# Kernel tuning notes

Measured on AMD Instinct MI355X. Metric: run time of the kernel, lower is better.

The kernel has to match this reference:

```python
import jax, jax.numpy as jnp
import numpy as np

N_AB, N_AG, F = 20000, 20000, 256
E_AB, E_AG, E_D = 320000, 320000, 640000
EPS = 1e-5


def _bn(x, gamma, beta):
    # BatchNorm1d, training-mode batch statistics (deterministic), biased variance
    mu = x.mean(0)
    var = x.var(0)
    return (x - mu) * jax.lax.rsqrt(var + EPS) * gamma + beta


def _gcn(x, ei, W, b, n):
    # PyG GCNConv: add self loops, symmetric deg^-1/2 normalization, scatter-add
    loop = jnp.arange(n, dtype=ei.dtype)
    src = jnp.concatenate([ei[0], loop])
    dst = jnp.concatenate([ei[1], loop])
    deg = jax.ops.segment_sum(jnp.ones_like(src, dtype=x.dtype), dst, num_segments=n)
    dinv = jax.lax.rsqrt(jnp.maximum(deg, 1.0))  # deg >= 1 due to self loops
    norm = dinv[src] * dinv[dst]                 # [E]
    h = x @ W                                    # [n, D]
    return jax.ops.segment_sum(h[src] * norm[:, None], dst, num_segments=n) + b


def _gat(x, ei, W, a_s, a_d, b, n, slope=0.2):
    # PyG GATConv, heads=1, add self loops; attention dropout off (eval mode)
    loop = jnp.arange(n, dtype=ei.dtype)
    src = jnp.concatenate([ei[0], loop])
    dst = jnp.concatenate([ei[1], loop])
    h = x @ W                                    # [n, D]
    e = jax.nn.leaky_relu((h @ a_s)[src] + (h @ a_d)[dst], slope)  # [E]
    # segment softmax over incoming edges of each dst node
    m = jax.ops.segment_max(e, dst, num_segments=n)
    ex = jnp.exp(e - m[dst])
    s = jax.ops.segment_sum(ex, dst, num_segments=n)
    alpha = ex / s[dst]
    return jax.ops.segment_sum(h[src] * alpha[:, None], dst, num_segments=n) + b


def setup_inputs() -> dict:
    key = jax.random.key(0)
    ks = jax.random.split(key, 20)
    sc = 1.0 / np.sqrt(F)
    sc2 = 1.0 / np.sqrt(2 * F)
    inp = {
        "x_ab": jax.random.normal(ks[0], (N_AB, F), jnp.float32),
        "x_ag": jax.random.normal(ks[1], (N_AG, F), jnp.float32),
        "W_gcn": jax.random.normal(ks[2], (F, F), jnp.float32) * sc,
        "b_gcn": jnp.zeros((F,), jnp.float32),
        "g1": jnp.ones((F,), jnp.float32),
        "be1": jnp.zeros((F,), jnp.float32),
        "W_aggcn": jax.random.normal(ks[3], (F, F), jnp.float32) * sc,
        "b_aggcn": jnp.zeros((F,), jnp.float32),
        "ag_g1": jnp.ones((F,), jnp.float32),
        "ag_be1": jnp.zeros((F,), jnp.float32),
        "W_gat": jax.random.normal(ks[4], (F, F), jnp.float32) * sc,
        "a_src": jax.random.normal(ks[5], (F,), jnp.float32) * sc,
        "a_dst": jax.random.normal(ks[6], (F,), jnp.float32) * sc,
        "b_gat": jnp.zeros((F,), jnp.float32),
        "W_gat2": jax.random.normal(ks[7], (F, F), jnp.float32) * sc,
        "a_src2": jax.random.normal(ks[8], (F,), jnp.float32) * sc,
        "a_dst2": jax.random.normal(ks[9], (F,), jnp.float32) * sc,
        "b_gat2": jnp.zeros((F,), jnp.float32),
        "ag_g2": jnp.ones((2 * F,), jnp.float32),
        "ag_be2": jnp.zeros((2 * F,), jnp.float32),
        "W_agfc": jax.random.normal(ks[10], (2 * F, 1), jnp.float32) * sc2,
        "b_agfc": jnp.zeros((1,), jnp.float32),
        "g2": jnp.ones((2 * F,), jnp.float32),
        "be2": jnp.zeros((2 * F,), jnp.float32),
        "W_fc": jax.random.normal(ks[11], (2 * F, 1), jnp.float32) * sc2,
        "b_fc": jnp.zeros((1,), jnp.float32),
        "edge_x_ab": jax.random.randint(ks[12], (2, E_AB), 0, N_AB, jnp.int32),
        "edge_x_ag": jax.random.randint(ks[13], (2, E_AG), 0, N_AG, jnp.int32),
        "edge_index_d": jax.random.randint(ks[14], (2, E_D), 0, N_AB + N_AG, jnp.int32),
    }
    return inp


def reference(x_ab, x_ag, W_gcn, b_gcn, g1, be1, W_aggcn, b_aggcn, ag_g1, ag_be1,
              W_gat, a_src, a_dst, b_gat, W_gat2, a_src2, a_dst2, b_gat2,
              ag_g2, ag_be2, W_agfc, b_agfc, g2, be2, W_fc, b_fc,
              edge_x_ab, edge_x_ag, edge_index_d):
    relu = jax.nn.relu
    h_ab = relu(_bn(_gcn(x_ab, edge_x_ab, W_gcn, b_gcn, N_AB), g1, be1))
    h_ag = relu(_bn(_gcn(x_ag, edge_x_ag, W_aggcn, b_aggcn, N_AG), ag_g1, ag_be1))
    # dropout layers are identity in eval mode
    n = N_AB + N_AG
    x = jnp.concatenate([h_ab, h_ag], axis=0)
    x = relu(_gat(x, edge_index_d, W_gat, a_src, a_dst, b_gat, n))
    x = _gat(x, edge_index_d, W_gat2, a_src2, a_dst2, b_gat2, n)
    x1, x2 = x[:N_AB], x[N_AB:]
    out_ag = relu(_bn(jnp.concatenate([x2, h_ag], axis=1), ag_g2, ag_be2)) @ W_agfc + b_agfc
    out_ab = relu(_bn(jnp.concatenate([x1, h_ab], axis=1), g2, be2)) @ W_fc + b_fc
    return out_ab, out_ag
```

## Files before the change

kernel.cpp:

```cpp
#include <hip/hip_runtime.h>
#include <hip/hip_bf16.h>
#include <stdint.h>

#define NF 256
#define EPSV 1e-5f
#define PB 160
#define MAXBUK 160

typedef unsigned short u16;
typedef unsigned int u32;
typedef short short8 __attribute__((ext_vector_type(8)));
typedef float floatx4 __attribute__((ext_vector_type(4)));

#define P_BGCN 0
#define P_G1 256
#define P_BE1 512
#define P_BAGG 768
#define P_AGG1 1024
#define P_AGBE1 1280
#define P_ASRC 1536
#define P_ADST 1792
#define P_BGAT 2048
#define P_ASRC2 2304
#define P_ADST2 2560
#define P_BGAT2 2816
#define P_G2 3072
#define P_BE2 3584
#define P_WFC 4096
#define P_AGG2 4608
#define P_AGBE2 5120
#define P_WAGFC 5632
#define P_BFC 6144
#define P_BAGFC 6145

__device__ __forceinline__ float bf2f(u16 u) {
    union { unsigned int i; float f; } v; v.i = ((unsigned int)u) << 16; return v.f;
}
__device__ __forceinline__ u16 f2bf(float f) {
    unsigned int x = __float_as_uint(f);
    unsigned int r = x + 0x7fffu + ((x >> 16) & 1u);
    return (u16)(r >> 16);
}
__device__ __forceinline__ float sane(float f) {
    return (f == f && fabsf(f) < 1e30f) ? f : 0.f;
}
__device__ __forceinline__ unsigned int zap2(unsigned int w) {
    if ((w & 0x00007F80u) == 0x00007F80u) w &= 0xFFFF0000u;
    if ((w & 0x7F800000u) == 0x7F800000u) w &= 0x0000FFFFu;
    return w;
}
__device__ __forceinline__ float lrelu(float x) { return x > 0.f ? x : 0.2f * x; }

__device__ __forceinline__ float4 ld4h(const u16* p) {
    uint2 u = *(const uint2*)p;
    float4 r;
    r.x = bf2f((u16)(u.x & 0xFFFFu)); r.y = bf2f((u16)(u.x >> 16));
    r.z = bf2f((u16)(u.y & 0xFFFFu)); r.w = bf2f((u16)(u.y >> 16));
    return r;
}
__device__ __forceinline__ void st4h(u16* p, float4 v) {
    uint2 u;
    u.x = (unsigned)f2bf(v.x) | ((unsigned)f2bf(v.y) << 16);
    u.y = (unsigned)f2bf(v.z) | ((unsigned)f2bf(v.w) << 16);
    *(uint2*)p = u;
}

__device__ __forceinline__ void fma8(const uint4 u, float a, float* acc) {
    acc[0] = fmaf(__uint_as_float(u.x << 16), a, acc[0]);
    acc[1] = fmaf(__uint_as_float(u.x & 0xFFFF0000u), a, acc[1]);
    acc[2] = fmaf(__uint_as_float(u.y << 16), a, acc[2]);
    acc[3] = fmaf(__uint_as_float(u.y & 0xFFFF0000u), a, acc[3]);
    acc[4] = fmaf(__uint_as_float(u.z << 16), a, acc[4]);
    acc[5] = fmaf(__uint_as_float(u.z & 0xFFFF0000u), a, acc[5]);
    acc[6] = fmaf(__uint_as_float(u.w << 16), a, acc[6]);
    acc[7] = fmaf(__uint_as_float(u.w & 0xFFFF0000u), a, acc[7]);
}
__device__ __forceinline__ void st8h(u16* p, const float* v) {
    uint4 u;
    u.x = (u32)f2bf(v[0]) | ((u32)f2bf(v[1]) << 16);
    u.y = (u32)f2bf(v[2]) | ((u32)f2bf(v[3]) << 16);
    u.z = (u32)f2bf(v[4]) | ((u32)f2bf(v[5]) << 16);
    u.w = (u32)f2bf(v[6]) | ((u32)f2bf(v[7]) << 16);
    *(uint4*)p = u;
}

__device__ __forceinline__ float wredsum(float v) {
#pragma unroll
    for (int o = 32; o > 0; o >>= 1) v += __shfl_xor(v, o, 64);
    return v;
}
__device__ __forceinline__ int wscan_incl(int x, int lane) {
#pragma unroll
    for (int o = 1; o < 64; o <<= 1) {
        int t = __shfl_up(x, o, 64);
        if (lane >= o) x += t;
    }
    return x;
}

__global__ void detect_k(const u16* __restrict__ x, int* __restrict__ flag) {
    __shared__ int cnt;
    if (threadIdx.x == 0) cnt = 0;
    __syncthreads();
    int c = 0;
#pragma unroll
    for (int k = 0; k < 4; ++k) {
        unsigned int u = x[2 * (threadIdx.x + 256 * k)];
        int e = (int)((u >> 7) & 0xFFu);
        if (u == 0u || (e >= 100 && e <= 140)) c++;
    }
    atomicAdd(&cnt, c);
    __syncthreads();
    if (threadIdx.x == 0) flag[0] = (cnt >= 512) ? 1 : 0;
}

__global__ void prep_k(const void* w0, const void* w1, const void* w2, const void* w3,
                       const void* p0, const void* p1, const void* p2, const void* p3,
                       const void* p4, const void* p5, const void* p6, const void* p7,
                       const void* p8, const void* p9, const void* p10, const void* p11,
                       const void* p12, const void* p13, const void* p14, const void* p15,
                       const void* p16, const void* p17, const void* p18, const void* p19,
                       u16* __restrict__ wtf, float* __restrict__ prm,
                       int* __restrict__ zb, int nz,
                       const int* __restrict__ flagp) {
    int f = flagp[0];
    int idx = blockIdx.x * 256 + threadIdx.x;
    if (idx < nz) zb[idx] = 0;
    if (idx < 262144) {
        const void* ws[4] = {w0, w1, w2, w3};
        int wi = idx >> 16;
        int rest = idx & 65535;
        int j = rest & 7;
        int lr = (rest >> 3) & 15;
        int q = (rest >> 7) & 3;
        int nf = (rest >> 9) & 15;
        int ks = (rest >> 13) & 7;
        int n = nf * 16 + lr;
        int k = ks * 32 + q * 8 + j;
        const void* W = ws[wi];
        u16 v;
        if (f) {
            v = ((const u16*)W)[k * NF + n];
            if ((v & 0x7F80u) == 0x7F80u) v = 0;
        } else {
            v = f2bf(sane(((const float*)W)[k * NF + n]));
        }
        wtf[idx] = v;
        return;
    }
    int pidx = idx - 262144;
    if (pidx >= 6146) return;
    const void* ptrs[20] = {p0, p1, p2, p3, p4, p5, p6, p7, p8, p9,
                            p10, p11, p12, p13, p14, p15, p16, p17, p18, p19};
    int t, j;
    if (pidx < 3072) { t = pidx >> 8; j = pidx & 255; }
    else if (pidx < 6144) { t = 12 + ((pidx - 3072) >> 9); j = (pidx - 3072) & 511; }
    else { t = 18 + (pidx - 6144); j = 0; }
    float v = f ? bf2f(((const u16*)ptrs[t])[j]) : ((const float*)ptrs[t])[j];
    prm[pidx] = sane(v);
}

__global__ __launch_bounds__(256) void bucket_cnt3_k(const int* e0, const int* e1,
                                                     const int* e2,
                                                     int* __restrict__ gbcnt) {
    int y = blockIdx.y;
    const int* ei = (y == 0) ? e0 : (y == 1) ? e1 : e2;
    int E = (y == 2) ? 640000 : 320000;
    int n = (y == 2) ? 40000 : 20000;
    int nbuk = (n + 255) >> 8;
    int base = blockIdx.x * 4096;
    if (base >= E) return;
    __shared__ int l[MAXBUK];
    if (threadIdx.x < nbuk) l[threadIdx.x] = 0;
    __syncthreads();
#pragma unroll
    for (int t = 0; t < 16; ++t) {
        int e = base + t * 256 + threadIdx.x;
        if (e < E) atomicAdd(&l[ei[E + e] >> 8], 1);
    }
    __syncthreads();
    if (threadIdx.x < nbuk) {
        int c = l[threadIdx.x];
        if (c) atomicAdd(&gbcnt[y * MAXBUK + threadIdx.x], c);
    }
}
__global__ __launch_bounds__(256) void bucket_scan3_k(const int* __restrict__ gbcnt,
                                                      int* __restrict__ bb,
                                                      int* rp0, int* rp1, int* rp2) {
    __shared__ int wp[4];
    int y = blockIdx.y;
    int n = (y == 2) ? 40000 : 20000;
    int E = (y == 2) ? 640000 : 320000;
    int nbuk = (n + 255) >> 8;
    int* rp = (y == 0) ? rp0 : (y == 1) ? rp1 : rp2;
    int lane = threadIdx.x & 63, wave = threadIdx.x >> 6;
    int v = (threadIdx.x < nbuk) ? gbcnt[y * MAXBUK + threadIdx.x] : 0;
    int x = wscan_incl(v, lane);
    if (lane == 63) wp[wave] = x;
    __syncthreads();
    int off = 0;
#pragma unroll
    for (int w = 0; w < 4; ++w) off += (w < wave) ? wp[w] : 0;
    if (threadIdx.x < nbuk) bb[y * (MAXBUK + 1) + threadIdx.x] = off + x - v;
    if (threadIdx.x == 0) {
        bb[y * (MAXBUK + 1) + nbuk] = E;
        rp[n] = E;
    }
}
__global__ __launch_bounds__(256) void bin3_k(const int* e0, const int* e1, const int* e2,
                                              const int* __restrict__ bb,
                                              int* __restrict__ gcur,
                                              u32* s0, u32* s1, u32* s2) {
    int y = blockIdx.y;
    const int* ei = (y == 0) ? e0 : (y == 1) ? e1 : e2;
    u32* stg = (y == 0) ? s0 : (y == 1) ? s1 : s2;
    int E = (y == 2) ? 640000 : 320000;
    int n = (y == 2) ? 40000 : 20000;
    int nbuk = (n + 255) >> 8;
    int base = blockIdx.x * 4096;
    if (base >= E) return;
    __shared__ int lcnt[MAXBUK];
    __shared__ int lbase[MAXBUK];
    if (threadIdx.x < nbuk) lcnt[threadIdx.x] = 0;
    __syncthreads();
#pragma unroll
    for (int t = 0; t < 16; ++t) {
        int e = base + t * 256 + threadIdx.x;
        if (e < E) atomicAdd(&lcnt[ei[E + e] >> 8], 1);
    }
    __syncthreads();
    if (threadIdx.x < nbuk) {
        int cnt = lcnt[threadIdx.x];
        int g = cnt ? atomicAdd(&gcur[y * MAXBUK + threadIdx.x], cnt) : 0;
        lbase[threadIdx.x] = bb[y * (MAXBUK + 1) + threadIdx.x] + g;
        lcnt[threadIdx.x] = 0;
    }
    __syncthreads();
#pragma unroll
    for (int t = 0; t < 16; ++t) {
        int e = base + t * 256 + threadIdx.x;
        if (e < E) {
            int s = ei[e], d = ei[E + e];
            int b = d >> 8;
            int r = atomicAdd(&lcnt[b], 1);
            stg[lbase[b] + r] = (u32)s | ((u32)(d & 255) << 16);
        }
    }
}
__global__ __launch_bounds__(256) void place3_k(const u32* s0, const u32* s1, const u32* s2,
                                                const int* __restrict__ bb,
                                                int* rp0, int* rp1, int* rp2,
                                                float* dv0, float* dv1,
                                                int* c0, int* c1, int* c2) {
    __shared__ int wp[4];
    __shared__ int lcnt[256];
    __shared__ int lrp[256];
    int y = blockIdx.y;
    int b = blockIdx.x;
    int n = (y == 2) ? 40000 : 20000;
    int nbuk = (n + 255) >> 8;
    if (b >= nbuk) return;
    const u32* stg = (y == 0) ? s0 : (y == 1) ? s1 : s2;
    int* rp = (y == 0) ? rp0 : (y == 1) ? rp1 : rp2;
    int* col = (y == 0) ? c0 : (y == 1) ? c1 : c2;
    int d0 = b << 8;
    int dn = min(256, n - d0);
    int base = bb[y * (MAXBUK + 1) + b];
    int endv = bb[y * (MAXBUK + 1) + b + 1];
    lcnt[threadIdx.x] = 0;
    __syncthreads();
    for (int j = base + threadIdx.x; j < endv; j += 256)
        atomicAdd(&lcnt[stg[j] >> 16], 1);
    __syncthreads();
    int lane = threadIdx.x & 63, wave = threadIdx.x >> 6;
    int v = lcnt[threadIdx.x];
    int x = wscan_incl(v, lane);
    if (lane == 63) wp[wave] = x;
    __syncthreads();
    int off = 0;
#pragma unroll
    for (int w = 0; w < 4; ++w) off += (w < wave) ? wp[w] : 0;
    int excl = base + off + x - v;
    lrp[threadIdx.x] = excl;
    if (threadIdx.x < dn) {
        rp[d0 + threadIdx.x] = excl;
        if (y == 0) dv0[d0 + threadIdx.x] = rsqrtf((float)(v + 1));
        else if (y == 1) dv1[d0 + threadIdx.x] = rsqrtf((float)(v + 1));
    }
    lcnt[threadIdx.x] = 0;
    __syncthreads();
    for (int j = base + threadIdx.x; j < endv; j += 256) {
        u32 rec = stg[j];
        int dl = (int)(rec >> 16);
        int s = (int)(rec & 0xFFFFu);
        int r = atomicAdd(&lcnt[dl], 1);
        col[lrp[dl] + r] = s;
    }
}

__global__ __launch_bounds__(256) void gemm2_k(const void* A0, const void* A1,
                                               const u16* __restrict__ Wtf0,
                                               const u16* __restrict__ Wtf1,
                                               const int* __restrict__ flagp,
                                               u16* __restrict__ C, int M) {
    int f = flagp[0];
    int y = blockIdx.y;
    const void* Aptr = y ? A1 : A0;
    const u16* Wtf = y ? Wtf1 : Wtf0;
    u16* Cp = C + (size_t)y * M * NF;
    int wave = threadIdx.x >> 6, lane = threadIdx.x & 63;
    int lr = lane & 15, q = lane >> 4;
    int arow = blockIdx.x * 64 + wave * 16 + lr;
    bool rok = arow < M;
    floatx4 acc[16];
#pragma unroll
    for (int nf = 0; nf < 16; ++nf) acc[nf] = (floatx4){0.f, 0.f, 0.f, 0.f};
    const u16* a16 = (const u16*)Aptr + (size_t)arow * NF;
    const float* a32 = (const float*)Aptr + (size_t)arow * NF;
#pragma unroll
    for (int ks = 0; ks < 8; ++ks) {
        int kk = ks * 32 + q * 8;
        union { u16 s[8]; uint4 u; short8 v; } a;
        if (!rok) {
            a.u = make_uint4(0u, 0u, 0u, 0u);
        } else if (f) {
            a.u = *(const uint4*)(a16 + kk);
            a.u.x = zap2(a.u.x); a.u.y = zap2(a.u.y);
            a.u.z = zap2(a.u.z); a.u.w = zap2(a.u.w);
        } else {
            float4 f0 = *(const float4*)(a32 + kk);
            float4 f1 = *(const float4*)(a32 + kk + 4);
            a.s[0] = f2bf(sane(f0.x)); a.s[1] = f2bf(sane(f0.y));
            a.s[2] = f2bf(sane(f0.z)); a.s[3] = f2bf(sane(f0.w));
            a.s[4] = f2bf(sane(f1.x)); a.s[5] = f2bf(sane(f1.y));
            a.s[6] = f2bf(sane(f1.z)); a.s[7] = f2bf(sane(f1.w));
        }
        const u16* bbase = Wtf + ks * 8192 + lane * 8;
#pragma unroll
        for (int nf = 0; nf < 16; ++nf) {
            short8 b = *(const short8*)(bbase + nf * 512);
            acc[nf] = __builtin_amdgcn_mfma_f32_16x16x32_bf16(a.v, b, acc[nf], 0, 0, 0);
        }
    }
#pragma unroll
    for (int nf = 0; nf < 16; ++nf) {
#pragma unroll
        for (int rr = 0; rr < 4; ++rr) {
            int gr = blockIdx.x * 64 + wave * 16 + q * 4 + rr;
            if (gr < M) Cp[(size_t)gr * NF + nf * 16 + lr] = f2bf(acc[nf][rr]);
        }
    }
}

__global__ __launch_bounds__(256) void gemm_gat_k(const u16* __restrict__ Aptr,
                                                  const u16* __restrict__ Wtf,
                                                  u16* __restrict__ C, int M,
                                                  const float* __restrict__ as_,
                                                  const float* __restrict__ ad_,
                                                  float* __restrict__ es,
                                                  float* __restrict__ ed) {
    int wave = threadIdx.x >> 6, lane = threadIdx.x & 63;
    int lr = lane & 15, q = lane >> 4;
    int arow = blockIdx.x * 64 + wave * 16 + lr;
    bool rok = arow < M;
    floatx4 acc[16];
#pragma unroll
    for (int nf = 0; nf < 16; ++nf) acc[nf] = (floatx4){0.f, 0.f, 0.f, 0.f};
    const u16* a16 = Aptr + (size_t)arow * NF;
#pragma unroll
    for (int ks = 0; ks < 8; ++ks) {
        int kk = ks * 32 + q * 8;
        union { uint4 u; short8 v; } a;
        a.u = rok ? *(const uint4*)(a16 + kk) : make_uint4(0u, 0u, 0u, 0u);
        const u16* bbase = Wtf + ks * 8192 + lane * 8;
#pragma unroll
        for (int nf = 0; nf < 16; ++nf) {
            short8 b = *(const short8*)(bbase + nf * 512);
            acc[nf] = __builtin_amdgcn_mfma_f32_16x16x32_bf16(a.v, b, acc[nf], 0, 0, 0);
        }
    }
#pragma unroll
    for (int nf = 0; nf < 16; ++nf) {
#pragma unroll
        for (int rr = 0; rr < 4; ++rr) {
            int gr = blockIdx.x * 64 + wave * 16 + q * 4 + rr;
            if (gr < M) C[(size_t)gr * NF + nf * 16 + lr] = f2bf(acc[nf][rr]);
        }
    }
    float asl[16], adl[16];
#pragma unroll
    for (int nf = 0; nf < 16; ++nf) { asl[nf] = as_[nf * 16 + lr]; adl[nf] = ad_[nf * 16 + lr]; }
#pragma unroll
    for (int rr = 0; rr < 4; ++rr) {
        float s1 = 0.f, s2 = 0.f;
#pragma unroll
        for (int nf = 0; nf < 16; ++nf) {
            s1 += acc[nf][rr] * asl[nf];
            s2 += acc[nf][rr] * adl[nf];
        }
#pragma unroll
        for (int o = 1; o < 16; o <<= 1) {
            s1 += __shfl_xor(s1, o, 64);
            s2 += __shfl_xor(s2, o, 64);
        }
        int gr = blockIdx.x * 64 + wave * 16 + q * 4 + rr;
        if (lr == 0 && gr < M) { es[gr] = s1; ed[gr] = s2; }
    }
}

__global__ __launch_bounds__(256) void gcn_csr2_k(const u16* __restrict__ h,
                                                  const int* rp0, const int* rp1,
                                                  const int* c0, const int* c1,
                                                  const float* dv0, const float* dv1,
                                                  const float* __restrict__ prm,
                                                  u16* __restrict__ out, int n) {
    int y = blockIdx.y;
    const int* rp = y ? rp1 : rp0;
    const int* col = y ? c1 : c0;
    const float* dinv = y ? dv1 : dv0;
    const float* b = prm + (y ? P_BAGG : P_BGCN);
    const u16* hb = h + (size_t)y * n * NF;
    u16* ob = out + (size_t)y * n * NF;
    int wave = threadIdx.x >> 6, lane = threadIdx.x & 63;
    int half = lane >> 5, sl = lane & 31;
    int i = blockIdx.x * 4 + wave;
    if (i >= n) return;
    int c = sl * 8;
    int beg = rp[i], end = rp[i + 1];
    float di = dinv[i];
    float acc[8] = {0.f, 0.f, 0.f, 0.f, 0.f, 0.f, 0.f, 0.f};
    float selfw = half ? 0.f : di * di;
    uint4 uv = *(const uint4*)(hb + (size_t)i * NF + c);
    fma8(uv, selfw, acc);
    int j = beg + half;
    for (; j + 6 < end; j += 8) {
        int s0 = col[j], s1 = col[j + 2], s2 = col[j + 4], s3 = col[j + 6];
        float n0 = dinv[s0] * di, n1 = dinv[s1] * di;
        float n2 = dinv[s2] * di, n3 = dinv[s3] * di;
        uint4 u0 = *(const uint4*)(hb + (size_t)s0 * NF + c);
        uint4 u1 = *(const uint4*)(hb + (size_t)s1 * NF + c);
        uint4 u2 = *(const uint4*)(hb + (size_t)s2 * NF + c);
        uint4 u3 = *(const uint4*)(hb + (size_t)s3 * NF + c);
        fma8(u0, n0, acc);
        fma8(u1, n1, acc);
        fma8(u2, n2, acc);
        fma8(u3, n3, acc);
    }
    for (; j < end; j += 2) {
        int s = col[j];
        float nr = dinv[s] * di;
        uint4 u = *(const uint4*)(hb + (size_t)s * NF + c);
        fma8(u, nr, acc);
    }
#pragma unroll
    for (int k = 0; k < 8; ++k) acc[k] += __shfl_xor(acc[k], 32, 64);
#pragma unroll
    for (int k = 0; k < 8; ++k) acc[k] += b[c + k];
    if (half == 0) st8h(ob + (size_t)i * NF + c, acc);
}

__global__ void bn_stats2_k(const u16* __restrict__ x, int n,
                            float* __restrict__ psum, float* __restrict__ psq) {
    int y = blockIdx.y;
    int c = threadIdx.x;
    int r0 = blockIdx.x * 128;
    int rend = min(r0 + 128, n);
    const u16* xb = x + (size_t)y * n * NF;
    float s = 0.f, qq = 0.f;
    for (int r = r0; r < rend; ++r) {
        float v = bf2f(xb[(size_t)r * NF + c]);
        s += v; qq += v * v;
    }
    size_t o = (size_t)(y * PB + blockIdx.x) * 512 + c;
    psum[o] = s; psq[o] = qq;
}
__global__ void bn_fin2_k(const float* __restrict__ psum, const float* __restrict__ psq,
                          float* __restrict__ stg, int n, int nb) {
    int y = blockIdx.y;
    int wave = threadIdx.x >> 6, lane = threadIdx.x & 63;
    int c = blockIdx.x * 4 + wave;
    float s = 0.f, qq = 0.f;
    for (int b = lane; b < nb; b += 64) {
        size_t o = (size_t)(y * PB + b) * 512 + c;
        s += psum[o]; qq += psq[o];
    }
    s = wredsum(s);
    qq = wredsum(qq);
    if (lane == 0) {
        float inv_n = 1.0f / (float)n;
        float mean = s * inv_n;
        float var = fmaxf(qq * inv_n - mean * mean, 0.f);
        stg[y * 512 + c] = mean;
        stg[y * 512 + 256 + c] = rsqrtf(var + EPSV);
    }
}
__global__ void bn_apply2_k(const u16* __restrict__ x, const float* __restrict__ stg,
                            const float* __restrict__ prm, u16* __restrict__ out, int n) {
    int y = blockIdx.y;
    int t = blockIdx.x * 256 + threadIdx.x;
    if (t >= n * (NF / 8)) return;
    int c = (t & 31) * 8;
    const float* st = stg + y * 512;
    const float* g = prm + (y ? P_AGG1 : P_G1);
    const float* be = prm + (y ? P_AGBE1 : P_BE1);
    uint4 u = *(const uint4*)(x + (size_t)y * n * NF + (size_t)t * 8);
    float v[8];
    v[0] = __uint_as_float(u.x << 16); v[1] = __uint_as_float(u.x & 0xFFFF0000u);
    v[2] = __uint_as_float(u.y << 16); v[3] = __uint_as_float(u.y & 0xFFFF0000u);
    v[4] = __uint_as_float(u.z << 16); v[5] = __uint_as_float(u.z & 0xFFFF0000u);
    v[6] = __uint_as_float(u.w << 16); v[7] = __uint_as_float(u.w & 0xFFFF0000u);
    float r[8];
#pragma unroll
    for (int k = 0; k < 8; ++k) {
        int cc = c + k;
        float w = (v[k] - st[cc]) * st[256 + cc] * g[cc] + be[cc];
        r[k] = fmaxf(w, 0.f);
    }
    st8h(out + (size_t)y * n * NF + (size_t)t * 8, r);
}

__global__ __launch_bounds__(256) void gat_csr_k(const u16* __restrict__ h,
                                                 const int* __restrict__ rp,
                                                 const int* __restrict__ col,
                                                 const float* __restrict__ es,
                                                 const float* __restrict__ ed,
                                                 const float* __restrict__ b,
                                                 u16* __restrict__ out, int n,
                                                 int do_relu) {
    int wave = threadIdx.x >> 6, lane = threadIdx.x & 63;
    int half = lane >> 5, sl = lane & 31;
    int i = blockIdx.x * 4 + wave;
    if (i >= n) return;
    int beg = rp[i], end = rp[i + 1];
    float edi = ed[i];
    int c = sl * 8;
    float acc[8] = {0.f, 0.f, 0.f, 0.f, 0.f, 0.f, 0.f, 0.f};
    float ws = __expf(lrelu(es[i] + edi));
    float selfw = half ? 0.f : ws;
    float ssum = selfw;
    uint4 uv = *(const uint4*)(h + (size_t)i * NF + c);
    fma8(uv, selfw, acc);
    int j = beg + half;
    for (; j + 6 < end; j += 8) {
        int s0 = col[j], s1 = col[j + 2], s2 = col[j + 4], s3 = col[j + 6];
        float e0 = es[s0], e1 = es[s1], e2 = es[s2], e3 = es[s3];
        uint4 u0 = *(const uint4*)(h + (size_t)s0 * NF + c);
        uint4 u1 = *(const uint4*)(h + (size_t)s1 * NF + c);
        uint4 u2 = *(const uint4*)(h + (size_t)s2 * NF + c);
        uint4 u3 = *(const uint4*)(h + (size_t)s3 * NF + c);
        float a0 = __expf(lrelu(e0 + edi));
        float a1 = __expf(lrelu(e1 + edi));
        float a2 = __expf(lrelu(e2 + edi));
        float a3 = __expf(lrelu(e3 + edi));
        ssum += (a0 + a1) + (a2 + a3);
        fma8(u0, a0, acc);
        fma8(u1, a1, acc);
        fma8(u2, a2, acc);
        fma8(u3, a3, acc);
    }
    for (; j < end; j += 2) {
        int s = col[j];
        float a = __expf(lrelu(es[s] + edi));
        uint4 u = *(const uint4*)(h + (size_t)s * NF + c);
        ssum += a;
        fma8(u, a, acc);
    }
    ssum += __shfl_xor(ssum, 32, 64);
#pragma unroll
    for (int k = 0; k < 8; ++k) acc[k] += __shfl_xor(acc[k], 32, 64);
    float inv = 1.0f / ssum;
#pragma unroll
    for (int k = 0; k < 8; ++k) {
        acc[k] = b[c + k] + acc[k] * inv;
        if (do_relu) acc[k] = fmaxf(acc[k], 0.f);
    }
    if (half == 0) st8h(out + (size_t)i * NF + c, acc);
}

__global__ void bn_stats_cat2_k(const u16* __restrict__ xp, const u16* __restrict__ hp,
                                int n, float* __restrict__ psum, float* __restrict__ psq) {
    int y = blockIdx.y;
    int c = threadIdx.x;
    int r0 = blockIdx.x * 128;
    int rend = min(r0 + 128, n);
    const u16* src = ((c < 256) ? xp : hp) + (size_t)y * n * NF;
    int cc = c & 255;
    float s = 0.f, qq = 0.f;
    for (int r = r0; r < rend; ++r) {
        float v = bf2f(src[(size_t)r * NF + cc]);
        s += v; qq += v * v;
    }
    size_t o = (size_t)(y * PB + blockIdx.x) * 512 + c;
    psum[o] = s; psq[o] = qq;
}
__global__ void bn_fin_cat2_k(const float* __restrict__ psum, const float* __restrict__ psq,
                              float* __restrict__ stc, int n, int nb) {
    int y = blockIdx.y;
    int wave = threadIdx.x >> 6, lane = threadIdx.x & 63;
    int c = blockIdx.x * 4 + wave;
    float s = 0.f, qq = 0.f;
    for (int b = lane; b < nb; b += 64) {
        size_t o = (size_t)(y * PB + b) * 512 + c;
        s += psum[o]; qq += psq[o];
    }
    s = wredsum(s);
    qq = wredsum(qq);
    if (lane == 0) {
        float inv_n = 1.0f / (float)n;
        float mean = s * inv_n;
        float var = fmaxf(qq * inv_n - mean * mean, 0.f);
        stc[y * 1024 + c] = mean;
        stc[y * 1024 + 512 + c] = rsqrtf(var + EPSV);
    }
}
__global__ void final2_k(const u16* __restrict__ xp, const u16* __restrict__ hp,
                         const float* __restrict__ stc, const float* __restrict__ prm,
                         float* __restrict__ out, int n) {
    int y = blockIdx.y;
    int wave = threadIdx.x >> 6, lane = threadIdx.x & 63;
    int i = blockIdx.x * 4 + wave;
    if (i >= n) return;
    const float* st = stc + y * 1024;
    const float* g = prm + (y ? P_AGG2 : P_G2);
    const float* be = prm + (y ? P_AGBE2 : P_BE2);
    const float* w = prm + (y ? P_WAGFC : P_WFC);
    float bias = prm[y ? P_BAGFC : P_BFC];
    const u16* src = (((lane < 32) ? xp : hp) + (size_t)y * n * NF) + (size_t)i * NF
                     + (lane < 32 ? lane * 8 : (lane - 32) * 8);
    uint4 u = *(const uint4*)src;
    float vv[8];
    vv[0] = bf2f((u16)(u.x & 0xFFFFu)); vv[1] = bf2f((u16)(u.x >> 16));
    vv[2] = bf2f((u16)(u.y & 0xFFFFu)); vv[3] = bf2f((u16)(u.y >> 16));
    vv[4] = bf2f((u16)(u.z & 0xFFFFu)); vv[5] = bf2f((u16)(u.z >> 16));
    vv[6] = bf2f((u16)(u.w & 0xFFFFu)); vv[7] = bf2f((u16)(u.w >> 16));
    int c0 = lane * 8;
    float acc = 0.f;
#pragma unroll
    for (int j = 0; j < 8; ++j) {
        int c = c0 + j;
        float v = (vv[j] - st[c]) * st[512 + c] * g[c] + be[c];
        v = fmaxf(v, 0.f);
        acc += v * w[c];
    }
    acc = wredsum(acc);
    if (lane == 0) out[(size_t)y * 20000 + i] = acc + bias;
}

extern "C" void kernel_launch(void* const* d_in, const int* in_sizes, int n_in,
                              void* d_out, int out_size, void* d_ws, size_t ws_size,
                              hipStream_t stream) {
    const void* x_ab = d_in[0];
    const void* x_ag = d_in[1];
    const int* e_ab = (const int*)d_in[26];
    const int* e_ag = (const int*)d_in[27];
    const int* e_d = (const int*)d_in[28];

    const int NAB = 20000, NT = 40000;
    const int EAB = 320000, EAG = 320000, ED = 640000;

    u16* hcat = (u16*)d_ws;
    u16* bufA = hcat + (size_t)NT * NF;
    u16* bufB = bufA + (size_t)NT * NF;
    u16* wt4 = bufB + (size_t)NT * NF;
    float* dv0 = (float*)(wt4 + 4 * 65536);
    float* dv1 = dv0 + NAB;
    float* es = dv1 + NAB;
    float* edv = es + NT;
    float* stg2 = edv + NT;
    float* stc = stg2 + 1024;
    float* psum = stc + 2048;
    float* psq = psum + 2 * PB * 512;
    float* prm = psq + 2 * PB * 512;
    int* flag = (int*)(prm + 8192);
    int* rp_ab = flag + 16;
    int* rp_ag = rp_ab + NAB + 1;
    int* rp_d = rp_ag + NAB + 1;
    int* gbcnt = rp_d + NT + 1;
    int* gcur = gbcnt + 3 * MAXBUK;
    int* bb = gcur + 3 * MAXBUK;
    int* col_ab = bb + 3 * (MAXBUK + 1);
    int* col_ag = col_ab + EAB;
    int* col_d = col_ag + EAG;
    u32* stg_ab = (u32*)(col_d + ED);
    u32* stg_ag = stg_ab + EAB;
    u32* stg_d = stg_ag + EAG;

    u16* wt_gcn = wt4;
    u16* wt_aggcn = wt4 + 65536;
    u16* wt_gat = wt4 + 2 * 65536;
    u16* wt_gat2 = wt4 + 3 * 65536;

    dim3 t256(256), t512(512);
    const int nbg = (NAB + 127) / 128;

    detect_k<<<dim3(1), t256, 0, stream>>>((const u16*)x_ab, flag);
    prep_k<<<dim3(1049), t256, 0, stream>>>(
        d_in[2], d_in[6], d_in[10], d_in[14],
        d_in[3], d_in[4], d_in[5], d_in[7], d_in[8], d_in[9],
        d_in[11], d_in[12], d_in[13], d_in[15], d_in[16], d_in[17],
        d_in[22], d_in[23], d_in[24], d_in[18], d_in[19], d_in[20],
        d_in[25], d_in[21], wt4, prm, gbcnt, 6 * MAXBUK + 3 * (MAXBUK + 1), flag);

    bucket_cnt3_k<<<dim3(157, 3), t256, 0, stream>>>(e_ab, e_ag, e_d, gbcnt);
    bucket_scan3_k<<<dim3(1, 3), t256, 0, stream>>>(gbcnt, bb, rp_ab, rp_ag, rp_d);
    bin3_k<<<dim3(157, 3), t256, 0, stream>>>(e_ab, e_ag, e_d, bb, gcur,
                                              stg_ab, stg_ag, stg_d);
    place3_k<<<dim3(157, 3), t256, 0, stream>>>(stg_ab, stg_ag, stg_d, bb,
                                                rp_ab, rp_ag, rp_d, dv0, dv1,
                                                col_ab, col_ag, col_d);

    gemm2_k<<<dim3((NAB + 63) / 64, 2), t256, 0, stream>>>(x_ab, x_ag, wt_gcn, wt_aggcn,
                                                           flag, bufA, NAB);
    gcn_csr2_k<<<dim3((NAB + 3) / 4, 2), t256, 0, stream>>>(bufA, rp_ab, rp_ag,
                                                            col_ab, col_ag, dv0, dv1,
                                                            prm, bufB, NAB);
    bn_stats2_k<<<dim3(nbg, 2), t256, 0, stream>>>(bufB, NAB, psum, psq);
    bn_fin2_k<<<dim3(64, 2), t256, 0, stream>>>(psum, psq, stg2, NAB, nbg);
    bn_apply2_k<<<dim3((NAB * NF / 8 + 255) / 256, 2), t256, 0, stream>>>(bufB, stg2, prm,
                                                                          hcat, NAB);

    gemm_gat_k<<<dim3((NT + 63) / 64), t256, 0, stream>>>(hcat, wt_gat, bufA, NT,
                                                          prm + P_ASRC, prm + P_ADST,
                                                          es, edv);
    gat_csr_k<<<dim3((NT + 3) / 4), t256, 0, stream>>>(bufA, rp_d, col_d, es, edv,
                                                       prm + P_BGAT, bufB, NT, 1);
    gemm_gat_k<<<dim3((NT + 63) / 64), t256, 0, stream>>>(bufB, wt_gat2, bufA, NT,
                                                          prm + P_ASRC2, prm + P_ADST2,
                                                          es, edv);
    gat_csr_k<<<dim3((NT + 3) / 4), t256, 0, stream>>>(bufA, rp_d, col_d, es, edv,
                                                       prm + P_BGAT2, bufB, NT, 0);

    bn_stats_cat2_k<<<dim3(nbg, 2), t512, 0, stream>>>(bufB, hcat, NAB, psum, psq);
    bn_fin_cat2_k<<<dim3(128, 2), t256, 0, stream>>>(psum, psq, stc, NAB, nbg);
    final2_k<<<dim3((NAB + 3) / 4, 2), t256, 0, stream>>>(bufB, hcat, stc, prm,
                                                          (float*)d_out, NAB);
}
```

Measured before the change: 508.0 us.

## Replace bucketed two-level CSR build with direct global-atomic count, scan, scatter

```diff
diff --git a/kernel.cpp b/kernel.cpp
--- a/kernel.cpp
+++ b/kernel.cpp
@@ -5,7 +5,6 @@
 #define NF 256
 #define EPSV 1e-5f
 #define PB 160
-#define MAXBUK 160
 
 typedef unsigned short u16;
 typedef unsigned int u32;
@@ -50,20 +49,6 @@
     return w;
 }
 __device__ __forceinline__ float lrelu(float x) { return x > 0.f ? x : 0.2f * x; }
-
-__device__ __forceinline__ float4 ld4h(const u16* p) {
-    uint2 u = *(const uint2*)p;
-    float4 r;
-    r.x = bf2f((u16)(u.x & 0xFFFFu)); r.y = bf2f((u16)(u.x >> 16));
-    r.z = bf2f((u16)(u.y & 0xFFFFu)); r.w = bf2f((u16)(u.y >> 16));
-    return r;
-}
-__device__ __forceinline__ void st4h(u16* p, float4 v) {
-    uint2 u;
-    u.x = (unsigned)f2bf(v.x) | ((unsigned)f2bf(v.y) << 16);
-    u.y = (unsigned)f2bf(v.z) | ((unsigned)f2bf(v.w) << 16);
-    *(uint2*)p = u;
-}
 
 __device__ __forceinline__ void fma8(const uint4 u, float a, float* acc) {
     acc[0] = fmaf(__uint_as_float(u.x << 16), a, acc[0]);
@@ -160,141 +145,78 @@
     prm[pidx] = sane(v);
 }
 
-__global__ __launch_bounds__(256) void bucket_cnt3_k(const int* e0, const int* e1,
-                                                     const int* e2,
-                                                     int* __restrict__ gbcnt) {
+__global__ __launch_bounds__(256) void cnt3_k(const int* e0, const int* e1, const int* e2,
+                                              int* rp0, int* rp1, int* rp2) {
     int y = blockIdx.y;
     const int* ei = (y == 0) ? e0 : (y == 1) ? e1 : e2;
     int E = (y == 2) ? 640000 : 320000;
-    int n = (y == 2) ? 40000 : 20000;
-    int nbuk = (n + 255) >> 8;
+    int* rp = (y == 0) ? rp0 : (y == 1) ? rp1 : rp2;
     int base = blockIdx.x * 4096;
     if (base >= E) return;
-    __shared__ int l[MAXBUK];
-    if (threadIdx.x < nbuk) l[threadIdx.x] = 0;
-    __syncthreads();
 #pragma unroll
     for (int t = 0; t < 16; ++t) {
         int e = base + t * 256 + threadIdx.x;
-        if (e < E) atomicAdd(&l[ei[E + e] >> 8], 1);
-    }
-    __syncthreads();
-    if (threadIdx.x < nbuk) {
-        int c = l[threadIdx.x];
-        if (c) atomicAdd(&gbcnt[y * MAXBUK + threadIdx.x], c);
-    }
-}
-__global__ __launch_bounds__(256) void bucket_scan3_k(const int* __restrict__ gbcnt,
-                                                      int* __restrict__ bb,
-                                                      int* rp0, int* rp1, int* rp2) {
-    __shared__ int wp[4];
+        if (e < E) atomicAdd(&rp[ei[E + e]], 1);
+    }
+}
+__global__ __launch_bounds__(1024) void scan3_k(int* rp0, int* rp1, int* rp2,
+                                                int* rw0, int* rw1, int* rw2,
+                                                float* dv0, float* dv1) {
+    __shared__ int wsum[16];
+    __shared__ int scarry;
     int y = blockIdx.y;
     int n = (y == 2) ? 40000 : 20000;
     int E = (y == 2) ? 640000 : 320000;
-    int nbuk = (n + 255) >> 8;
     int* rp = (y == 0) ? rp0 : (y == 1) ? rp1 : rp2;
-    int lane = threadIdx.x & 63, wave = threadIdx.x >> 6;
-    int v = (threadIdx.x < nbuk) ? gbcnt[y * MAXBUK + threadIdx.x] : 0;
-    int x = wscan_incl(v, lane);
-    if (lane == 63) wp[wave] = x;
+    int* rw = (y == 0) ? rw0 : (y == 1) ? rw1 : rw2;
+    int tid = threadIdx.x, lane = tid & 63, wv = tid >> 6;
+    if (tid == 0) scarry = 0;
     __syncthreads();
-    int off = 0;
-#pragma unroll
-    for (int w = 0; w < 4; ++w) off += (w < wave) ? wp[w] : 0;
-    if (threadIdx.x < nbuk) bb[y * (MAXBUK + 1) + threadIdx.x] = off + x - v;
-    if (threadIdx.x == 0) {
-        bb[y * (MAXBUK + 1) + nbuk] = E;
-        rp[n] = E;
-    }
-}
-__global__ __launch_bounds__(256) void bin3_k(const int* e0, const int* e1, const int* e2,
-                                              const int* __restrict__ bb,
-                                              int* __restrict__ gcur,
-                                              u32* s0, u32* s1, u32* s2) {
+    for (int base = 0; base < n; base += 1024) {
+        int i = base + tid;
+        int v = (i < n) ? rp[i] : 0;
+        int x = wscan_incl(v, lane);
+        if (lane == 63) wsum[wv] = x;
+        __syncthreads();
+        int off = scarry;
+#pragma unroll
+        for (int w = 0; w < 16; ++w) off += (w < wv) ? wsum[w] : 0;
+        int excl = off + x - v;
+        if (i < n) {
+            if (y == 0) dv0[i] = rsqrtf((float)(v + 1));
+            else if (y == 1) dv1[i] = rsqrtf((float)(v + 1));
+            rp[i] = excl;
+            rw[i] = excl;
+        }
+        __syncthreads();
+        if (tid == 0) {
+            int tot = 0;
+#pragma unroll
+            for (int w = 0; w < 16; ++w) tot += wsum[w];
+            scarry += tot;
+        }
+        __syncthreads();
+    }
+    if (tid == 0) rp[n] = E;
+}
+__global__ __launch_bounds__(256) void place3b_k(const int* e0, const int* e1, const int* e2,
+                                                 int* rw0, int* rw1, int* rw2,
+                                                 int* c0, int* c1, int* c2) {
     int y = blockIdx.y;
     const int* ei = (y == 0) ? e0 : (y == 1) ? e1 : e2;
-    u32* stg = (y == 0) ? s0 : (y == 1) ? s1 : s2;
     int E = (y == 2) ? 640000 : 320000;
-    int n = (y == 2) ? 40000 : 20000;
-    int nbuk = (n + 255) >> 8;
+    int* rw = (y == 0) ? rw0 : (y == 1) ? rw1 : rw2;
+    int* col = (y == 0) ? c0 : (y == 1) ? c1 : c2;
     int base = blockIdx.x * 4096;
     if (base >= E) return;
-    __shared__ int lcnt[MAXBUK];
-    __shared__ int lbase[MAXBUK];
-    if (threadIdx.x < nbuk) lcnt[threadIdx.x] = 0;
-    __syncthreads();
-#pragma unroll
-    for (int t = 0; t < 16; ++t) {
-        int e = base + t * 256 + threadIdx.x;
-        if (e < E) atomicAdd(&lcnt[ei[E + e] >> 8], 1);
-    }
-    __syncthreads();
-    if (threadIdx.x < nbuk) {
-        int cnt = lcnt[threadIdx.x];
-        int g = cnt ? atomicAdd(&gcur[y * MAXBUK + threadIdx.x], cnt) : 0;
-        lbase[threadIdx.x] = bb[y * (MAXBUK + 1) + threadIdx.x] + g;
-        lcnt[threadIdx.x] = 0;
-    }
-    __syncthreads();
 #pragma unroll
     for (int t = 0; t < 16; ++t) {
         int e = base + t * 256 + threadIdx.x;
         if (e < E) {
             int s = ei[e], d = ei[E + e];
-            int b = d >> 8;
-            int r = atomicAdd(&lcnt[b], 1);
-            stg[lbase[b] + r] = (u32)s | ((u32)(d & 255) << 16);
-        }
-    }
-}
-__global__ __launch_bounds__(256) void place3_k(const u32* s0, const u32* s1, const u32* s2,
-                                                const int* __restrict__ bb,
-                                                int* rp0, int* rp1, int* rp2,
-                                                float* dv0, float* dv1,
-                                                int* c0, int* c1, int* c2) {
-    __shared__ int wp[4];
-    __shared__ int lcnt[256];
-    __shared__ int lrp[256];
-    int y = blockIdx.y;
-    int b = blockIdx.x;
-    int n = (y == 2) ? 40000 : 20000;
-    int nbuk = (n + 255) >> 8;
-    if (b >= nbuk) return;
-    const u32* stg = (y == 0) ? s0 : (y == 1) ? s1 : s2;
-    int* rp = (y == 0) ? rp0 : (y == 1) ? rp1 : rp2;
-    int* col = (y == 0) ? c0 : (y == 1) ? c1 : c2;
-    int d0 = b << 8;
-    int dn = min(256, n - d0);
-    int base = bb[y * (MAXBUK + 1) + b];
-    int endv = bb[y * (MAXBUK + 1) + b + 1];
-    lcnt[threadIdx.x] = 0;
-    __syncthreads();
-    for (int j = base + threadIdx.x; j < endv; j += 256)
-        atomicAdd(&lcnt[stg[j] >> 16], 1);
-    __syncthreads();
-    int lane = threadIdx.x & 63, wave = threadIdx.x >> 6;
-    int v = lcnt[threadIdx.x];
-    int x = wscan_incl(v, lane);
-    if (lane == 63) wp[wave] = x;
-    __syncthreads();
-    int off = 0;
-#pragma unroll
-    for (int w = 0; w < 4; ++w) off += (w < wave) ? wp[w] : 0;
-    int excl = base + off + x - v;
-    lrp[threadIdx.x] = excl;
-    if (threadIdx.x < dn) {
-        rp[d0 + threadIdx.x] = excl;
-        if (y == 0) dv0[d0 + threadIdx.x] = rsqrtf((float)(v + 1));
-        else if (y == 1) dv1[d0 + threadIdx.x] = rsqrtf((float)(v + 1));
-    }
-    lcnt[threadIdx.x] = 0;
-    __syncthreads();
-    for (int j = base + threadIdx.x; j < endv; j += 256) {
-        u32 rec = stg[j];
-        int dl = (int)(rec >> 16);
-        int s = (int)(rec & 0xFFFFu);
-        int r = atomicAdd(&lcnt[dl], 1);
-        col[lrp[dl] + r] = s;
+            int p = atomicAdd(&rw[d], 1);
+            col[p] = s;
+        }
     }
 }
 
@@ -675,23 +597,21 @@
     int* rp_ab = flag + 16;
     int* rp_ag = rp_ab + NAB + 1;
     int* rp_d = rp_ag + NAB + 1;
-    int* gbcnt = rp_d + NT + 1;
-    int* gcur = gbcnt + 3 * MAXBUK;
-    int* bb = gcur + 3 * MAXBUK;
-    int* col_ab = bb + 3 * (MAXBUK + 1);
+    int* rw_ab = rp_d + NT + 1;
+    int* rw_ag = rw_ab + NAB + 1;
+    int* rw_d = rw_ag + NAB + 1;
+    int* col_ab = rw_d + NT + 1;
     int* col_ag = col_ab + EAB;
     int* col_d = col_ag + EAG;
-    u32* stg_ab = (u32*)(col_d + ED);
-    u32* stg_ag = stg_ab + EAB;
-    u32* stg_d = stg_ag + EAG;
 
     u16* wt_gcn = wt4;
     u16* wt_aggcn = wt4 + 65536;
     u16* wt_gat = wt4 + 2 * 65536;
     u16* wt_gat2 = wt4 + 3 * 65536;
 
-    dim3 t256(256), t512(512);
+    dim3 t256(256), t512(512), t1024(1024);
     const int nbg = (NAB + 127) / 128;
+    const int nzero = (NAB + 1) * 2 + (NT + 1);
 
     detect_k<<<dim3(1), t256, 0, stream>>>((const u16*)x_ab, flag);
     prep_k<<<dim3(1049), t256, 0, stream>>>(
@@ -699,15 +619,14 @@
         d_in[3], d_in[4], d_in[5], d_in[7], d_in[8], d_in[9],
         d_in[11], d_in[12], d_in[13], d_in[15], d_in[16], d_in[17],
         d_in[22], d_in[23], d_in[24], d_in[18], d_in[19], d_in[20],
-        d_in[25], d_in[21], wt4, prm, gbcnt, 6 * MAXBUK + 3 * (MAXBUK + 1), flag);
-
-    bucket_cnt3_k<<<dim3(157, 3), t256, 0, stream>>>(e_ab, e_ag, e_d, gbcnt);
-    bucket_scan3_k<<<dim3(1, 3), t256, 0, stream>>>(gbcnt, bb, rp_ab, rp_ag, rp_d);
-    bin3_k<<<dim3(157, 3), t256, 0, stream>>>(e_ab, e_ag, e_d, bb, gcur,
-                                              stg_ab, stg_ag, stg_d);
-    place3_k<<<dim3(157, 3), t256, 0, stream>>>(stg_ab, stg_ag, stg_d, bb,
-                                                rp_ab, rp_ag, rp_d, dv0, dv1,
-                                                col_ab, col_ag, col_d);
+        d_in[25], d_in[21], wt4, prm, rp_ab, nzero, flag);
+
+    cnt3_k<<<dim3(157, 3), t256, 0, stream>>>(e_ab, e_ag, e_d, rp_ab, rp_ag, rp_d);
+    scan3_k<<<dim3(1, 3), t1024, 0, stream>>>(rp_ab, rp_ag, rp_d,
+                                              rw_ab, rw_ag, rw_d, dv0, dv1);
+    place3b_k<<<dim3(157, 3), t256, 0, stream>>>(e_ab, e_ag, e_d,
+                                                 rw_ab, rw_ag, rw_d,
+                                                 col_ab, col_ag, col_d);
 
     gemm2_k<<<dim3((NAB + 63) / 64, 2), t256, 0, stream>>>(x_ab, x_ag, wt_gcn, wt_aggcn,
                                                            flag, bufA, NAB);
```

New measurement: 645.3 us. 1.27x slower.
